# Kernel tuning notes

Measured on AMD Instinct MI355X. Metric: run time of the kernel, lower is better.

## Reference

```python
import jax, jax.numpy as jnp
import numpy as np


def conv1x1(x, w, b):
    # x: [B,Ci,H,W], w: [Co,Ci,1,1], b: [Co]
    return jnp.einsum('bihw,oi->bohw', x, w[:, :, 0, 0]) + b[None, :, None, None]


def guide_nn(x, w1, b1, w2, b2):
    h = jax.nn.relu(conv1x1(x, w1, b1))
    return jnp.tanh(conv1x1(h, w2, b2))


def trilinear_slice(grid, gx, gy, gz):
    # grid: [B,C,D,Gh,Gw]; gx,gy,gz: [B,H,W] in ~[-1,1]
    B, C, D, Gh, Gw = grid.shape
    fx = jnp.clip((gx + 1.0) * 0.5 * (Gw - 1), 0.0, Gw - 1)
    fy = jnp.clip((gy + 1.0) * 0.5 * (Gh - 1), 0.0, Gh - 1)
    fz = jnp.clip((gz + 1.0) * 0.5 * (D - 1), 0.0, D - 1)
    x0 = jnp.floor(fx).astype(jnp.int32); x1 = jnp.minimum(x0 + 1, Gw - 1)
    y0 = jnp.floor(fy).astype(jnp.int32); y1 = jnp.minimum(y0 + 1, Gh - 1)
    z0 = jnp.floor(fz).astype(jnp.int32); z1 = jnp.minimum(z0 + 1, D - 1)
    wx = (fx - x0)[:, None]; wy = (fy - y0)[:, None]; wz = (fz - z0)[:, None]

    gather = jax.vmap(lambda g, zi, yi, xi: g[:, zi, yi, xi])  # -> [B,C,H,W]

    out = (
        gather(grid, z0, y0, x0) * (1 - wz) * (1 - wy) * (1 - wx)
        + gather(grid, z0, y0, x1) * (1 - wz) * (1 - wy) * wx
        + gather(grid, z0, y1, x0) * (1 - wz) * wy * (1 - wx)
        + gather(grid, z0, y1, x1) * (1 - wz) * wy * wx
        + gather(grid, z1, y0, x0) * wz * (1 - wy) * (1 - wx)
        + gather(grid, z1, y0, x1) * wz * (1 - wy) * wx
        + gather(grid, z1, y1, x0) * wz * wy * (1 - wx)
        + gather(grid, z1, y1, x1) * wz * wy * wx
    )
    return out


def slicing(grid, guide):
    # guide: [B,1,H,W] (single-channel context map)
    B, c, H, W = guide.shape
    x = (jnp.arange(W, dtype=guide.dtype) - W / 2) / (W / 2)
    y = (jnp.arange(H, dtype=guide.dtype) - H / 2) / (H / 2)
    yy, xx = jnp.meshgrid(y, x, indexing='ij')
    gx = jnp.broadcast_to(xx[None], (B, H, W))
    gy = jnp.broadcast_to(yy[None], (B, H, W))
    gz = guide[:, 0]
    return trilinear_slice(grid, gx, gy, gz)


def apply_coefficent(x, coeff):
    # x: [B,Ci,H,W]; coeff: [B,Co,Ci+1,H,W] -> per-pixel affine
    ci = x.shape[1]
    return jnp.einsum('boihw,bihw->bohw', coeff[:, :, :ci], x) + coeff[:, :, ci]


def setup_inputs() -> dict:
    key = jax.random.key(0)
    ks = jax.random.split(key, 12)
    B, H, W = 8, 512, 512
    D, Gh, Gw = 8, 16, 16
    inp = {
        'src': jax.random.uniform(ks[0], (B, 3, H, W), jnp.float32),
        'grid1': jax.random.normal(ks[1], (B, 32, D, Gh, Gw), jnp.float32),
        'grid2': jax.random.normal(ks[2], (B, 27, D, Gh, Gw), jnp.float32),
        'w1': jax.random.normal(ks[3], (16, 3, 1, 1), jnp.float32) * 0.1,
        'b1': jnp.zeros((16,), jnp.float32),
        'w2': jax.random.normal(ks[4], (1, 16, 1, 1), jnp.float32) * 0.1,
        'b2': jnp.zeros((1,), jnp.float32),
        'w3': jax.random.normal(ks[5], (16, 8, 1, 1), jnp.float32) * 0.1,
        'b3': jnp.zeros((16,), jnp.float32),
        'w4': jax.random.normal(ks[6], (1, 16, 1, 1), jnp.float32) * 0.1,
        'b4': jnp.zeros((1,), jnp.float32),
    }
    return inp


def reference(src, grid1, grid2, w1, b1, w2, b2, w3, b3, w4, b4):
    B, _, H, W = src.shape
    context_map = guide_nn(src, w1, b1, w2, b2)            # [B,1,H,W]
    coeff1 = slicing(grid1, context_map)                    # [B,32,H,W]
    coeff1_split = jnp.transpose(coeff1.reshape(B, 4, 8, H, W), (0, 2, 1, 3, 4))  # [B,8,4,H,W]
    hidden = jax.nn.relu(apply_coefficent(src, coeff1_split))  # [B,8,H,W]
    context_map2 = guide_nn(hidden, w3, b3, w4, b4)         # [B,1,H,W]
    coeff2 = slicing(grid2, context_map2)                   # [B,27,H,W]
    coeff2_split = jnp.transpose(coeff2.reshape(B, 9, 3, H, W), (0, 2, 1, 3, 4))  # [B,3,9,H,W]
    out = apply_coefficent(hidden, coeff2_split)            # [B,3,H,W]
    return out
```

## Files before the change

kernel.cpp:

```cpp
#include <hip/hip_runtime.h>
#include <math.h>

#define BATCH 8
#define IMH 512
#define IMW 512
#define HWSZ (IMH * IMW)
#define XSPAN 9
#define CPAD 36
#define L_CELLS (XSPAN * 8)
#define LSLOT (L_CELLS * CPAD)

__device__ __forceinline__ float fast_tanh(float x) {
    float e = __expf(2.0f * x);
    return fmaf(-2.0f, __builtin_amdgcn_rcpf(e + 1.0f), 1.0f);
}

__global__ __launch_bounds__(256) void transpose_both(const float* __restrict__ g1,
                                                      const float* __restrict__ g2,
                                                      float* __restrict__ t1,
                                                      float* __restrict__ t2) {
    int idx = blockIdx.x * 256 + threadIdx.x;
    if (idx < 524288) {
        int x = idx & 15, y = (idx >> 4) & 15, z = (idx >> 8) & 7;
        int c = (idx >> 11) & 31, b = idx >> 16;
        t1[((((b * 16 + y) * 16 + x) * 8 + z) << 5) + c] = g1[idx];
    } else if (idx < 966656) {
        int j = idx - 524288;
        int x = j & 15, y = (j >> 4) & 15, z = (j >> 8) & 7;
        int r = j >> 11;
        int c = r % 27, b = r / 27;
        t2[(((b * 16 + y) * 16 + x) * 8 + z) * 28 + c] = g2[j];
    } else {
        int k = idx - 966656;
        t2[k * 28 + 27] = 0.0f;
    }
}

template <bool TR>
__global__ __launch_bounds__(256, 4) void fused2(
    const float* __restrict__ src,
    const float* __restrict__ g1p,
    const float* __restrict__ g2p,
    const float* __restrict__ w1, const float* __restrict__ b1,
    const float* __restrict__ w2, const float* __restrict__ b2,
    const float* __restrict__ w3, const float* __restrict__ b3,
    const float* __restrict__ w4, const float* __restrict__ b4,
    float* __restrict__ out) {
    __shared__ __align__(16) float L1s[LSLOT];
    __shared__ __align__(16) float L2s[LSLOT];

    int tid = threadIdx.x;
    int half = blockIdx.x & 1;
    int h = (blockIdx.x >> 1) & 511;
    int b = blockIdx.x >> 10;
    int w0 = half << 8;
    int x_lo = half ? 7 : 0;

    float fy = (float)h * (15.0f / 512.0f);
    int y0 = (int)fy;
    float wy = fy - (float)y0;
    int y1 = y0 + 1;

    if (TR) {
        const float* p1a = g1p + ((((size_t)b * 16 + y0) * 16 + x_lo) * 8) * 32;
        const float* p1b = g1p + ((((size_t)b * 16 + y1) * 16 + x_lo) * 8) * 32;
        for (int t = tid; t < L_CELLS * 8; t += 256) {
            int g = t & 7, cell = t >> 3;
            float4 v0 = *(const float4*)(p1a + (size_t)t * 4);
            float4 v1 = *(const float4*)(p1b + (size_t)t * 4);
            float4 r;
            r.x = fmaf(wy, v1.x - v0.x, v0.x);
            r.y = fmaf(wy, v1.y - v0.y, v0.y);
            r.z = fmaf(wy, v1.z - v0.z, v0.z);
            r.w = fmaf(wy, v1.w - v0.w, v0.w);
            *(float4*)&L1s[cell * CPAD + 4 * g] = r;
        }
        const float* p2a = g2p + ((((size_t)b * 16 + y0) * 16 + x_lo) * 8) * 28;
        const float* p2b = g2p + ((((size_t)b * 16 + y1) * 16 + x_lo) * 8) * 28;
        for (int t = tid; t < L_CELLS * 7; t += 256) {
            int g = t % 7, cell = t / 7;
            float4 v0 = *(const float4*)(p2a + (size_t)t * 4);
            float4 v1 = *(const float4*)(p2b + (size_t)t * 4);
            float4 r;
            r.x = fmaf(wy, v1.x - v0.x, v0.x);
            r.y = fmaf(wy, v1.y - v0.y, v0.y);
            r.z = fmaf(wy, v1.z - v0.z, v0.z);
            r.w = fmaf(wy, v1.w - v0.w, v0.w);
            *(float4*)&L2s[cell * CPAD + 4 * g] = r;
        }
    } else {
        for (int t = tid; t < L_CELLS * 32; t += 256) {
            int c = t & 31, cell = t >> 5;
            int z = cell & 7, xj = cell >> 3;
            size_t o0 = ((((size_t)b * 32 + c) * 8 + z) * 16 + y0) * 16 + (x_lo + xj);
            float v0 = g1p[o0], v1 = g1p[o0 + 16];
            L1s[cell * CPAD + c] = fmaf(wy, v1 - v0, v0);
        }
        for (int t = tid; t < L_CELLS * 28; t += 256) {
            int c = t % 28, cell = t / 28;
            int z = cell & 7, xj = cell >> 3;
            float v = 0.0f;
            if (c < 27) {
                size_t o0 = ((((size_t)b * 27 + c) * 8 + z) * 16 + y0) * 16 + (x_lo + xj);
                v = fmaf(wy, g2p[o0 + 16] - g2p[o0], g2p[o0]);
            }
            L2s[cell * CPAD + c] = v;
        }
    }
    __syncthreads();

    int w = w0 + tid;
    const float* sb = src + (size_t)b * 3 * HWSZ + h * IMW + w;
    float s0 = sb[0];
    float s1 = sb[HWSZ];
    float s2 = sb[2 * HWSZ];

    float acc = b2[0];
#pragma unroll
    for (int j = 0; j < 16; ++j) {
        float t = fmaf(w1[j * 3 + 0], s0,
                  fmaf(w1[j * 3 + 1], s1,
                  fmaf(w1[j * 3 + 2], s2, b1[j])));
        acc = fmaf(w2[j], fmaxf(t, 0.0f), acc);
    }
    float fz = fmaf(fast_tanh(acc), 3.5f, 3.5f);
    fz = fminf(fmaxf(fz, 0.0f), 7.0f);
    int z0 = min((int)fz, 6);
    float wz = fz - (float)z0;

    float fx = (float)w * (15.0f / 512.0f);
    int x0 = (int)fx;
    float wx = fx - (float)x0;
    int a00 = ((x0 - x_lo) * 8 + z0) * CPAD;

    float w11v = wx * wz;
    float w10v = wx - w11v;
    float w01v = wz - w11v;
    float w00v = 1.0f - wx - wz + w11v;

    float c1[32];
#pragma unroll
    for (int i = 0; i < 8; ++i) {
        float4 v00 = *(const float4*)&L1s[a00 + 4 * i];
        float4 v01 = *(const float4*)&L1s[a00 + CPAD + 4 * i];
        float4 v10 = *(const float4*)&L1s[a00 + 8 * CPAD + 4 * i];
        float4 v11 = *(const float4*)&L1s[a00 + 9 * CPAD + 4 * i];
        c1[4 * i + 0] = fmaf(v00.x, w00v, fmaf(v01.x, w01v, fmaf(v10.x, w10v, v11.x * w11v)));
        c1[4 * i + 1] = fmaf(v00.y, w00v, fmaf(v01.y, w01v, fmaf(v10.y, w10v, v11.y * w11v)));
        c1[4 * i + 2] = fmaf(v00.z, w00v, fmaf(v01.z, w01v, fmaf(v10.z, w10v, v11.z * w11v)));
        c1[4 * i + 3] = fmaf(v00.w, w00v, fmaf(v01.w, w01v, fmaf(v10.w, w10v, v11.w * w11v)));
    }

    float hid[8];
#pragma unroll
    for (int o = 0; o < 8; ++o) {
        float t = fmaf(c1[o], s0,
                  fmaf(c1[8 + o], s1,
                  fmaf(c1[16 + o], s2, c1[24 + o])));
        hid[o] = fmaxf(t, 0.0f);
    }

    float acc2 = b4[0];
#pragma unroll
    for (int j = 0; j < 16; ++j) {
        float t = b3[j];
#pragma unroll
        for (int i = 0; i < 8; ++i) t = fmaf(w3[j * 8 + i], hid[i], t);
        acc2 = fmaf(w4[j], fmaxf(t, 0.0f), acc2);
    }
    float fz2 = fmaf(fast_tanh(acc2), 3.5f, 3.5f);
    fz2 = fminf(fmaxf(fz2, 0.0f), 7.0f);
    int z0b = min((int)fz2, 6);
    float wz2 = fz2 - (float)z0b;

    int a00b = ((x0 - x_lo) * 8 + z0b) * CPAD;
    float u11 = wx * wz2;
    float u10 = wx - u11;
    float u01 = wz2 - u11;
    float u00 = 1.0f - wx - wz2 + u11;

    float c2[28];
#pragma unroll
    for (int i = 0; i < 7; ++i) {
        float4 v00 = *(const float4*)&L2s[a00b + 4 * i];
        float4 v01 = *(const float4*)&L2s[a00b + CPAD + 4 * i];
        float4 v10 = *(const float4*)&L2s[a00b + 8 * CPAD + 4 * i];
        float4 v11 = *(const float4*)&L2s[a00b + 9 * CPAD + 4 * i];
        c2[4 * i + 0] = fmaf(v00.x, u00, fmaf(v01.x, u01, fmaf(v10.x, u10, v11.x * u11)));
        c2[4 * i + 1] = fmaf(v00.y, u00, fmaf(v01.y, u01, fmaf(v10.y, u10, v11.y * u11)));
        c2[4 * i + 2] = fmaf(v00.z, u00, fmaf(v01.z, u01, fmaf(v10.z, u10, v11.z * u11)));
        c2[4 * i + 3] = fmaf(v00.w, u00, fmaf(v01.w, u01, fmaf(v10.w, u10, v11.w * u11)));
    }

    float* ob = out + (size_t)b * 3 * HWSZ + h * IMW + w;
#pragma unroll
    for (int o = 0; o < 3; ++o) {
        float t = c2[24 + o];
#pragma unroll
        for (int i = 0; i < 8; ++i) t = fmaf(c2[i * 3 + o], hid[i], t);
        ob[(size_t)o * HWSZ] = t;
    }
}

extern "C" void kernel_launch(void* const* d_in, const int* in_sizes, int n_in,
                              void* d_out, int out_size, void* d_ws, size_t ws_size,
                              hipStream_t stream) {
    const float* src   = (const float*)d_in[0];
    const float* grid1 = (const float*)d_in[1];
    const float* grid2 = (const float*)d_in[2];
    const float* w1 = (const float*)d_in[3];
    const float* b1 = (const float*)d_in[4];
    const float* w2 = (const float*)d_in[5];
    const float* b2 = (const float*)d_in[6];
    const float* w3 = (const float*)d_in[7];
    const float* b3 = (const float*)d_in[8];
    const float* w4 = (const float*)d_in[9];
    const float* b4 = (const float*)d_in[10];
    float* out = (float*)d_out;

    const size_t t1_elems = 524288;
    const size_t t2_elems = (size_t)8 * 2048 * 28;
    const size_t ws_needed = (t1_elems + t2_elems) * sizeof(float);

    const int nblk = (BATCH * HWSZ) / 256;

    if (ws_size >= ws_needed) {
        float* t1 = (float*)d_ws;
        float* t2 = t1 + t1_elems;
        transpose_both<<<3840, 256, 0, stream>>>(grid1, grid2, t1, t2);
        fused2<true><<<nblk, 256, 0, stream>>>(
            src, t1, t2, w1, b1, w2, b2, w3, b3, w4, b4, out);
    } else {
        fused2<false><<<nblk, 256, 0, stream>>>(
            src, grid1, grid2, w1, b1, w2, b2, w3, b3, w4, b4, out);
    }
}
```

Before: 133.9 us.

## Store sliced bilateral grids in fp16 and interpolate with packed half math

```diff
diff --git a/kernel.cpp b/kernel.cpp
--- a/kernel.cpp
+++ b/kernel.cpp
@@ -6,9 +6,13 @@
 #define IMW 512
 #define HWSZ (IMH * IMW)
 #define XSPAN 9
-#define CPAD 36
+#define CH 32
+#define CPADH 40
 #define L_CELLS (XSPAN * 8)
-#define LSLOT (L_CELLS * CPAD)
+#define LSLOTH (L_CELLS * CPADH)
+
+typedef _Float16 half1;
+typedef _Float16 half8 __attribute__((ext_vector_type(8)));
 
 __device__ __forceinline__ float fast_tanh(float x) {
     float e = __expf(2.0f * x);
@@ -17,94 +21,95 @@
 
 __global__ __launch_bounds__(256) void transpose_both(const float* __restrict__ g1,
                                                       const float* __restrict__ g2,
-                                                      float* __restrict__ t1,
-                                                      float* __restrict__ t2) {
+                                                      half1* __restrict__ t1,
+                                                      half1* __restrict__ t2) {
     int idx = blockIdx.x * 256 + threadIdx.x;
     if (idx < 524288) {
         int x = idx & 15, y = (idx >> 4) & 15, z = (idx >> 8) & 7;
         int c = (idx >> 11) & 31, b = idx >> 16;
-        t1[((((b * 16 + y) * 16 + x) * 8 + z) << 5) + c] = g1[idx];
+        t1[((((b * 16 + y) * 16 + x) * 8 + z) << 5) + c] = (half1)g1[idx];
     } else if (idx < 966656) {
         int j = idx - 524288;
         int x = j & 15, y = (j >> 4) & 15, z = (j >> 8) & 7;
         int r = j >> 11;
         int c = r % 27, b = r / 27;
-        t2[(((b * 16 + y) * 16 + x) * 8 + z) * 28 + c] = g2[j];
+        t2[((((b * 16 + y) * 16 + x) * 8 + z) << 5) + c] = (half1)g2[j];
     } else {
         int k = idx - 966656;
-        t2[k * 28 + 27] = 0.0f;
+        int cell = k / 5, p = k - cell * 5;
+        t2[(cell << 5) + 27 + p] = (half1)0.0f;
     }
 }
 
 template <bool TR>
-__global__ __launch_bounds__(256, 4) void fused2(
+__global__ __launch_bounds__(256, 4) void fused3(
     const float* __restrict__ src,
-    const float* __restrict__ g1p,
-    const float* __restrict__ g2p,
+    const void* __restrict__ g1p,
+    const void* __restrict__ g2p,
     const float* __restrict__ w1, const float* __restrict__ b1,
     const float* __restrict__ w2, const float* __restrict__ b2,
     const float* __restrict__ w3, const float* __restrict__ b3,
     const float* __restrict__ w4, const float* __restrict__ b4,
     float* __restrict__ out) {
-    __shared__ __align__(16) float L1s[LSLOT];
-    __shared__ __align__(16) float L2s[LSLOT];
+    __shared__ __align__(16) half1 L1h[LSLOTH];
+    __shared__ __align__(16) half1 L2h[LSLOTH];
 
     int tid = threadIdx.x;
-    int half = blockIdx.x & 1;
+    int half_ = blockIdx.x & 1;
     int h = (blockIdx.x >> 1) & 511;
     int b = blockIdx.x >> 10;
-    int w0 = half << 8;
-    int x_lo = half ? 7 : 0;
+    int w0 = half_ << 8;
+    int x_lo = half_ ? 7 : 0;
 
     float fy = (float)h * (15.0f / 512.0f);
     int y0 = (int)fy;
     float wy = fy - (float)y0;
-    int y1 = y0 + 1;
 
     if (TR) {
-        const float* p1a = g1p + ((((size_t)b * 16 + y0) * 16 + x_lo) * 8) * 32;
-        const float* p1b = g1p + ((((size_t)b * 16 + y1) * 16 + x_lo) * 8) * 32;
-        for (int t = tid; t < L_CELLS * 8; t += 256) {
-            int g = t & 7, cell = t >> 3;
-            float4 v0 = *(const float4*)(p1a + (size_t)t * 4);
-            float4 v1 = *(const float4*)(p1b + (size_t)t * 4);
-            float4 r;
-            r.x = fmaf(wy, v1.x - v0.x, v0.x);
-            r.y = fmaf(wy, v1.y - v0.y, v0.y);
-            r.z = fmaf(wy, v1.z - v0.z, v0.z);
-            r.w = fmaf(wy, v1.w - v0.w, v0.w);
-            *(float4*)&L1s[cell * CPAD + 4 * g] = r;
-        }
-        const float* p2a = g2p + ((((size_t)b * 16 + y0) * 16 + x_lo) * 8) * 28;
-        const float* p2b = g2p + ((((size_t)b * 16 + y1) * 16 + x_lo) * 8) * 28;
-        for (int t = tid; t < L_CELLS * 7; t += 256) {
-            int g = t % 7, cell = t / 7;
-            float4 v0 = *(const float4*)(p2a + (size_t)t * 4);
-            float4 v1 = *(const float4*)(p2b + (size_t)t * 4);
-            float4 r;
-            r.x = fmaf(wy, v1.x - v0.x, v0.x);
-            r.y = fmaf(wy, v1.y - v0.y, v0.y);
-            r.z = fmaf(wy, v1.z - v0.z, v0.z);
-            r.w = fmaf(wy, v1.w - v0.w, v0.w);
-            *(float4*)&L2s[cell * CPAD + 4 * g] = r;
+        half1 wyh = (half1)wy;
+        const half1* t1h = (const half1*)g1p;
+        const half1* t2h = (const half1*)g2p;
+        {
+            const half8* pa = (const half8*)(t1h + ((((size_t)b * 16 + y0) * 16 + x_lo) * 8) * CH);
+            const half8* pb = pa + (16 * 8 * CH) / 8;
+            for (int t = tid; t < L_CELLS * 4; t += 256) {
+                int g = t & 3, cell = t >> 2;
+                half8 v0 = pa[t];
+                half8 v1 = pb[t];
+                half8 r = v0 + (v1 - v0) * wyh;
+                *(half8*)&L1h[cell * CPADH + 8 * g] = r;
+            }
+        }
+        {
+            const half8* pa = (const half8*)(t2h + ((((size_t)b * 16 + y0) * 16 + x_lo) * 8) * CH);
+            const half8* pb = pa + (16 * 8 * CH) / 8;
+            for (int t = tid; t < L_CELLS * 4; t += 256) {
+                int g = t & 3, cell = t >> 2;
+                half8 v0 = pa[t];
+                half8 v1 = pb[t];
+                half8 r = v0 + (v1 - v0) * wyh;
+                *(half8*)&L2h[cell * CPADH + 8 * g] = r;
+            }
         }
     } else {
-        for (int t = tid; t < L_CELLS * 32; t += 256) {
+        const float* g1f = (const float*)g1p;
+        const float* g2f = (const float*)g2p;
+        for (int t = tid; t < L_CELLS * CH; t += 256) {
             int c = t & 31, cell = t >> 5;
             int z = cell & 7, xj = cell >> 3;
             size_t o0 = ((((size_t)b * 32 + c) * 8 + z) * 16 + y0) * 16 + (x_lo + xj);
-            float v0 = g1p[o0], v1 = g1p[o0 + 16];
-            L1s[cell * CPAD + c] = fmaf(wy, v1 - v0, v0);
-        }
-        for (int t = tid; t < L_CELLS * 28; t += 256) {
-            int c = t % 28, cell = t / 28;
+            float v0 = g1f[o0], v1 = g1f[o0 + 16];
+            L1h[cell * CPADH + c] = (half1)fmaf(wy, v1 - v0, v0);
+        }
+        for (int t = tid; t < L_CELLS * CH; t += 256) {
+            int c = t & 31, cell = t >> 5;
             int z = cell & 7, xj = cell >> 3;
             float v = 0.0f;
             if (c < 27) {
                 size_t o0 = ((((size_t)b * 27 + c) * 8 + z) * 16 + y0) * 16 + (x_lo + xj);
-                v = fmaf(wy, g2p[o0 + 16] - g2p[o0], g2p[o0]);
+                v = fmaf(wy, g2f[o0 + 16] - g2f[o0], g2f[o0]);
             }
-            L2s[cell * CPAD + c] = v;
+            L2h[cell * CPADH + c] = (half1)v;
         }
     }
     __syncthreads();
@@ -131,32 +136,32 @@
     float fx = (float)w * (15.0f / 512.0f);
     int x0 = (int)fx;
     float wx = fx - (float)x0;
-    int a00 = ((x0 - x_lo) * 8 + z0) * CPAD;
+    int a00 = ((x0 - x_lo) * 8 + z0) * CPADH;
 
     float w11v = wx * wz;
     float w10v = wx - w11v;
     float w01v = wz - w11v;
     float w00v = 1.0f - wx - wz + w11v;
-
-    float c1[32];
-#pragma unroll
-    for (int i = 0; i < 8; ++i) {
-        float4 v00 = *(const float4*)&L1s[a00 + 4 * i];
-        float4 v01 = *(const float4*)&L1s[a00 + CPAD + 4 * i];
-        float4 v10 = *(const float4*)&L1s[a00 + 8 * CPAD + 4 * i];
-        float4 v11 = *(const float4*)&L1s[a00 + 9 * CPAD + 4 * i];
-        c1[4 * i + 0] = fmaf(v00.x, w00v, fmaf(v01.x, w01v, fmaf(v10.x, w10v, v11.x * w11v)));
-        c1[4 * i + 1] = fmaf(v00.y, w00v, fmaf(v01.y, w01v, fmaf(v10.y, w10v, v11.y * w11v)));
-        c1[4 * i + 2] = fmaf(v00.z, w00v, fmaf(v01.z, w01v, fmaf(v10.z, w10v, v11.z * w11v)));
-        c1[4 * i + 3] = fmaf(v00.w, w00v, fmaf(v01.w, w01v, fmaf(v10.w, w10v, v11.w * w11v)));
+    half1 w00h = (half1)w00v, w01h = (half1)w01v, w10h = (half1)w10v, w11h = (half1)w11v;
+
+    const half8* q00 = (const half8*)&L1h[a00];
+    const half8* q01 = (const half8*)&L1h[a00 + CPADH];
+    const half8* q10 = (const half8*)&L1h[a00 + 8 * CPADH];
+    const half8* q11 = (const half8*)&L1h[a00 + 9 * CPADH];
+    float c1f[32];
+#pragma unroll
+    for (int j = 0; j < 4; ++j) {
+        half8 A = q00[j] * w00h + q01[j] * w01h + q10[j] * w10h + q11[j] * w11h;
+#pragma unroll
+        for (int k = 0; k < 8; ++k) c1f[j * 8 + k] = (float)A[k];
     }
 
     float hid[8];
 #pragma unroll
     for (int o = 0; o < 8; ++o) {
-        float t = fmaf(c1[o], s0,
-                  fmaf(c1[8 + o], s1,
-                  fmaf(c1[16 + o], s2, c1[24 + o])));
+        float t = fmaf(c1f[o], s0,
+                  fmaf(c1f[8 + o], s1,
+                  fmaf(c1f[16 + o], s2, c1f[24 + o])));
         hid[o] = fmaxf(t, 0.0f);
     }
 
@@ -173,31 +178,32 @@
     int z0b = min((int)fz2, 6);
     float wz2 = fz2 - (float)z0b;
 
-    int a00b = ((x0 - x_lo) * 8 + z0b) * CPAD;
+    int a00b = ((x0 - x_lo) * 8 + z0b) * CPADH;
     float u11 = wx * wz2;
     float u10 = wx - u11;
     float u01 = wz2 - u11;
     float u00 = 1.0f - wx - wz2 + u11;
-
-    float c2[28];
-#pragma unroll
-    for (int i = 0; i < 7; ++i) {
-        float4 v00 = *(const float4*)&L2s[a00b + 4 * i];
-        float4 v01 = *(const float4*)&L2s[a00b + CPAD + 4 * i];
-        float4 v10 = *(const float4*)&L2s[a00b + 8 * CPAD + 4 * i];
-        float4 v11 = *(const float4*)&L2s[a00b + 9 * CPAD + 4 * i];
-        c2[4 * i + 0] = fmaf(v00.x, u00, fmaf(v01.x, u01, fmaf(v10.x, u10, v11.x * u11)));
-        c2[4 * i + 1] = fmaf(v00.y, u00, fmaf(v01.y, u01, fmaf(v10.y, u10, v11.y * u11)));
-        c2[4 * i + 2] = fmaf(v00.z, u00, fmaf(v01.z, u01, fmaf(v10.z, u10, v11.z * u11)));
-        c2[4 * i + 3] = fmaf(v00.w, u00, fmaf(v01.w, u01, fmaf(v10.w, u10, v11.w * u11)));
+    half1 u00h = (half1)u00, u01h = (half1)u01, u10h = (half1)u10, u11h = (half1)u11;
+
+    const half8* r00 = (const half8*)&L2h[a00b];
+    const half8* r01 = (const half8*)&L2h[a00b + CPADH];
+    const half8* r10 = (const half8*)&L2h[a00b + 8 * CPADH];
+    const half8* r11 = (const half8*)&L2h[a00b + 9 * CPADH];
+    float c2f[27];
+#pragma unroll
+    for (int j = 0; j < 4; ++j) {
+        half8 A = r00[j] * u00h + r01[j] * u01h + r10[j] * u10h + r11[j] * u11h;
+#pragma unroll
+        for (int k = 0; k < 8; ++k)
+            if (j * 8 + k < 27) c2f[j * 8 + k] = (float)A[k];
     }
 
     float* ob = out + (size_t)b * 3 * HWSZ + h * IMW + w;
 #pragma unroll
     for (int o = 0; o < 3; ++o) {
-        float t = c2[24 + o];
-#pragma unroll
-        for (int i = 0; i < 8; ++i) t = fmaf(c2[i * 3 + o], hid[i], t);
+        float t = c2f[24 + o];
+#pragma unroll
+        for (int i = 0; i < 8; ++i) t = fmaf(c2f[i * 3 + o], hid[i], t);
         ob[(size_t)o * HWSZ] = t;
     }
 }
@@ -218,20 +224,19 @@
     const float* b4 = (const float*)d_in[10];
     float* out = (float*)d_out;
 
-    const size_t t1_elems = 524288;
-    const size_t t2_elems = (size_t)8 * 2048 * 28;
-    const size_t ws_needed = (t1_elems + t2_elems) * sizeof(float);
+    const size_t t_elems = (size_t)BATCH * 2048 * CH;
+    const size_t ws_needed = 2 * t_elems * sizeof(half1);
 
     const int nblk = (BATCH * HWSZ) / 256;
 
     if (ws_size >= ws_needed) {
-        float* t1 = (float*)d_ws;
-        float* t2 = t1 + t1_elems;
-        transpose_both<<<3840, 256, 0, stream>>>(grid1, grid2, t1, t2);
-        fused2<true><<<nblk, 256, 0, stream>>>(
+        half1* t1 = (half1*)d_ws;
+        half1* t2 = t1 + t_elems;
+        transpose_both<<<4096, 256, 0, stream>>>(grid1, grid2, t1, t2);
+        fused3<true><<<nblk, 256, 0, stream>>>(
             src, t1, t2, w1, b1, w2, b2, w3, b3, w4, b4, out);
     } else {
-        fused2<false><<<nblk, 256, 0, stream>>>(
+        fused3<false><<<nblk, 256, 0, stream>>>(
             src, grid1, grid2, w1, b1, w2, b2, w3, b3, w4, b4, out);
     }
 }
```

After: 146.9 us. +9.7%, slower.
